# Performance work log

Measured on AMD Instinct MI355X. Metric: run time of the kernel, lower is better.

## Reference

```python
import jax, jax.numpy as jnp
import numpy as np

N_NODES = 50000
N_REL = 4
N_EDGES = 800000
IN_DIM = 128
HID = 128
N_CLASSES = 16


def setup_inputs() -> dict:
    key = jax.random.key(0)
    ks = jax.random.split(key, 12)
    feat = jax.random.normal(ks[0], (N_NODES, IN_DIM), dtype=jnp.float32)
    src = jax.random.randint(ks[1], (N_REL, N_EDGES), 0, N_NODES, dtype=jnp.int32)
    dst = jax.random.randint(ks[2], (N_REL, N_EDGES), 0, N_NODES, dtype=jnp.int32)
    s = 0.05
    W1 = jax.random.normal(ks[3], (N_REL, IN_DIM, HID), dtype=jnp.float32) * s
    b1 = jax.random.normal(ks[4], (N_REL, HID), dtype=jnp.float32) * s
    W2 = jax.random.normal(ks[5], (N_REL, HID, HID), dtype=jnp.float32) * s
    b2 = jax.random.normal(ks[6], (N_REL, HID), dtype=jnp.float32) * s
    W3 = jax.random.normal(ks[7], (N_REL, HID, HID), dtype=jnp.float32) * s
    b3 = jax.random.normal(ks[8], (N_REL, HID), dtype=jnp.float32) * s
    Wlin = jax.random.normal(ks[9], (HID, N_CLASSES), dtype=jnp.float32) * s
    blin = jax.random.normal(ks[10], (N_CLASSES,), dtype=jnp.float32) * s
    return {"feat": feat, "src": src, "dst": dst, "W1": W1, "b1": b1,
            "W2": W2, "b2": b2, "W3": W3, "b3": b3, "Wlin": Wlin, "blin": blin}


def _graph_conv(x, s, d, W, b, n_nodes):
    """DGL GraphConv with norm='both': D_dst^-1/2 * A * D_src^-1/2 * x, then @W + b."""
    ones = jnp.ones(s.shape[0], dtype=x.dtype)
    deg_out = jnp.maximum(jax.ops.segment_sum(ones, s, num_segments=n_nodes), 1.0)
    deg_in = jnp.maximum(jax.ops.segment_sum(ones, d, num_segments=n_nodes), 1.0)
    xs = x * (deg_out ** -0.5)[:, None]          # [N, F]
    agg = jax.ops.segment_sum(xs[s], d, num_segments=n_nodes)  # gather+scatter [N, F]
    agg = agg * (deg_in ** -0.5)[:, None]
    return agg @ W + b


def _hetero_layer(x, src, dst, W, b, n_nodes):
    # HeteroGraphConv aggregate='sum' over relations (loop over small fixed R)
    out = _graph_conv(x, src[0], dst[0], W[0], b[0], n_nodes)
    for r in range(1, src.shape[0]):
        out = out + _graph_conv(x, src[r], dst[r], W[r], b[r], n_nodes)
    return out


def _l2_normalize(x, eps=1e-12):
    # torch F.normalize: x / max(||x||_2, eps), per row
    nrm = jnp.sqrt(jnp.sum(x * x, axis=1, keepdims=True))
    return x / jnp.maximum(nrm, eps)


def reference(feat, src, dst, W1, b1, W2, b2, W3, b3, Wlin, blin):
    n = feat.shape[0]
    h = _hetero_layer(feat, src, dst, W1, b1, n)
    h = jax.nn.leaky_relu(_l2_normalize(h), negative_slope=0.01)
    h = _hetero_layer(h, src, dst, W2, b2, n)
    h = jax.nn.leaky_relu(_l2_normalize(h), negative_slope=0.01)
    h = _hetero_layer(h, src, dst, W3, b3, n)
    # update_all(copy_u, sum) across all relations (unnormalized scatter-sum)
    pooled = jax.ops.segment_sum(h[src[0]], dst[0], num_segments=n)
    for r in range(1, src.shape[0]):
        pooled = pooled + jax.ops.segment_sum(h[src[r]], dst[r], num_segments=n)
    hg = jnp.mean(pooled, axis=0, keepdims=True)  # dgl.mean_nodes -> [1, HID]
    return jax.nn.sigmoid(hg @ Wlin + blin)       # [1, n_classes]
```

## Files before the change

### kernel.cpp

```cpp
#include <hip/hip_runtime.h>
#include <hip/hip_bf16.h>

constexpr int N_NODES = 50000;
constexpr int N_REL   = 4;
constexpr int N_EDGES = 800000;
constexpr int DIM     = 128;
constexpr int N_CLS   = 16;

constexpr int CHUNK  = 256;
constexpr int NCHUNK = (N_NODES + CHUNK - 1) / CHUNK;
constexpr int NPART  = N_REL * NCHUNK;

constexpr int NCBR  = (N_NODES + 255) / 256;
constexpr int NCB   = N_REL * NCBR;
constexpr int TILE  = 8000;
constexpr int TPR   = N_EDGES / TILE;
constexpr int MAXB  = 6144;

constexpr int RNG    = 12544;
constexpr int NRANGE = 4;
constexpr int DTILE  = 80000;
constexpr int DNT    = N_EDGES / DTILE;

constexpr int NPB = 8;

constexpr float YSCALE = 32.0f;

typedef __attribute__((ext_vector_type(8))) short short8;
typedef __attribute__((ext_vector_type(4))) float float4v;
typedef __attribute__((ext_vector_type(2))) float floatx2;

__device__ __forceinline__ unsigned int f2bf_bits(float f) {
  unsigned int u = __float_as_uint(f);
  return (u + 0x7fffu + ((u >> 16) & 1u)) >> 16;
}
__device__ __forceinline__ unsigned int pack2bf(float a, float b) {
  return f2bf_bits(a) | (f2bf_bits(b) << 16);
}

__device__ __forceinline__ int LCOL(int p) { return (p & 7) * 16 + (p >> 3); }

__global__ __launch_bounds__(256) void degree_hist(
    const int* __restrict__ src, const int* __restrict__ dst,
    int* __restrict__ cnt_out, int* __restrict__ cnt_in) {
  int b = blockIdx.x;
  int t     = b % DNT;    b /= DNT;
  int range = b % NRANGE; b /= NRANGE;
  int r     = b % N_REL;  b /= N_REL;
  int which = b;
  const int* arr = (which ? dst : src) + (size_t)r * N_EDGES + (size_t)t * DTILE;
  int* cnt = (which ? cnt_in : cnt_out) + r * N_NODES;
  int tid = threadIdx.x;
  __shared__ int h[RNG];
  for (int i = tid; i < RNG; i += 256) h[i] = 0;
  __syncthreads();
  int lo = range * RNG;
  int hi = lo + RNG;
  const int4* a4 = (const int4*)arr;
  for (int i = tid; i < DTILE / 4; i += 256) {
    int4 v = a4[i];
    if (v.x >= lo && v.x < hi) atomicAdd(&h[v.x - lo], 1);
    if (v.y >= lo && v.y < hi) atomicAdd(&h[v.y - lo], 1);
    if (v.z >= lo && v.z < hi) atomicAdd(&h[v.z - lo], 1);
    if (v.w >= lo && v.w < hi) atomicAdd(&h[v.w - lo], 1);
  }
  __syncthreads();
  for (int i = tid; i < RNG; i += 256) {
    int n = lo + i;
    int c = h[i];
    if (n < N_NODES && c) atomicAdd(&cnt[n], c);
  }
}

__global__ __launch_bounds__(256) void scan_partial(
    const int* __restrict__ cnt_in, int* __restrict__ partial) {
  int b = blockIdx.x;
  int r = b / NCHUNK, c = b % NCHUNK;
  int i = c * CHUNK + threadIdx.x;
  int v = (i < N_NODES) ? cnt_in[r * N_NODES + i] : 0;
#pragma unroll
  for (int off = 1; off < 64; off <<= 1) v += __shfl_xor(v, off, 64);
  __shared__ int ws[4];
  if ((threadIdx.x & 63) == 0) ws[threadIdx.x >> 6] = v;
  __syncthreads();
  if (threadIdx.x == 0) partial[b] = ws[0] + ws[1] + ws[2] + ws[3];
}

__global__ __launch_bounds__(1024) void scan_offsets(
    const int* __restrict__ partial, int* __restrict__ chunk_off,
    int* __restrict__ row_ptr) {
  __shared__ int lds[1024];
  __shared__ int sexcl[1024];
  __shared__ int stotal;
  int tid = threadIdx.x;
  int v = (tid < NPART) ? partial[tid] : 0;
  lds[tid] = v;
  __syncthreads();
  for (int off = 1; off < 1024; off <<= 1) {
    int t = (tid >= off) ? lds[tid - off] : 0;
    __syncthreads();
    lds[tid] += t;
    __syncthreads();
  }
  int excl = lds[tid] - v;
  sexcl[tid] = excl;
  if (tid == NPART - 1) stotal = excl + v;
  if (tid < NPART) chunk_off[tid] = excl;
  __syncthreads();
  if (tid < N_REL) {
    int base = sexcl[tid * NCHUNK];
    int next = (tid < N_REL - 1) ? sexcl[(tid + 1) * NCHUNK] : stotal;
    row_ptr[tid * (N_NODES + 1) + N_NODES] = next - base;
  }
}

__global__ __launch_bounds__(256) void scan_expand(
    const int* __restrict__ cnt_in, const int* __restrict__ chunk_off,
    int* __restrict__ row_ptr, int* __restrict__ cbcur) {
  int b = blockIdx.x;
  int r = b / NCHUNK, c = b % NCHUNK;
  int tid = threadIdx.x;
  int i = c * CHUNK + tid;
  int v = (i < N_NODES) ? cnt_in[r * N_NODES + i] : 0;
  __shared__ int lds[CHUNK];
  lds[tid] = v;
  __syncthreads();
  for (int off = 1; off < CHUNK; off <<= 1) {
    int t = (tid >= off) ? lds[tid - off] : 0;
    __syncthreads();
    lds[tid] += t;
    __syncthreads();
  }
  int excl = lds[tid] - v;
  int base = chunk_off[b] - chunk_off[r * NCHUNK];
  if (i < N_NODES) row_ptr[r * (N_NODES + 1) + i] = base + excl;
  if (tid == 0) cbcur[r * NCBR + c] = base;
}

__global__ __launch_bounds__(256) void pass1_bin(
    const int* __restrict__ src, const int* __restrict__ dst,
    int* __restrict__ cbcur, unsigned int* __restrict__ binned) {
  int b = blockIdx.x;
  int r = b / TPR, t = b % TPR;
  const int* sp = src + (size_t)r * N_EDGES + t * TILE;
  const int* dp = dst + (size_t)r * N_EDGES + t * TILE;
  unsigned int* outp = binned + (size_t)r * N_EDGES;
  int tid = threadIdx.x;
  __shared__ int hist[NCBR];
  __shared__ int scanb[256];
  __shared__ int gbase[NCBR];
  __shared__ int lcur[NCBR];
  for (int i = tid; i < NCBR; i += 256) hist[i] = 0;
  __syncthreads();
  for (int i = tid; i < TILE; i += 256) atomicAdd(&hist[dp[i] >> 8], 1);
  __syncthreads();
  int v = (tid < NCBR) ? hist[tid] : 0;
  scanb[tid] = v;
  __syncthreads();
  for (int off = 1; off < 256; off <<= 1) {
    int tv = (tid >= off) ? scanb[tid - off] : 0;
    __syncthreads();
    scanb[tid] += tv;
    __syncthreads();
  }
  if (tid < NCBR) {
    int excl = scanb[tid] - v;
    gbase[tid] = atomicAdd(&cbcur[r * NCBR + tid], v) - excl;
    lcur[tid] = excl;
  }
  __syncthreads();
  for (int i = tid; i < TILE; i += 256) {
    int d = dp[i];
    int s = sp[i];
    int cb = d >> 8;
    int lp = atomicAdd(&lcur[cb], 1);
    outp[gbase[cb] + lp] = ((unsigned)s << 8) | (unsigned)(d & 255);
  }
}

__global__ __launch_bounds__(256) void pass2_sort(
    const unsigned int* __restrict__ binned, const int* __restrict__ row_ptr,
    unsigned short* __restrict__ csr) {
  int b = blockIdx.x;
  int r = b / NCBR, c = b % NCBR;
  int node0 = c * 256;
  int node1 = min(node0 + 256, N_NODES);
  int start = row_ptr[r * (N_NODES + 1) + node0];
  int endv  = row_ptr[r * (N_NODES + 1) + node1];
  int count = endv - start;
  const unsigned int* bp = binned + (size_t)r * N_EDGES + start;
  unsigned short* outg = csr + (size_t)r * N_EDGES + start;
  int tid = threadIdx.x;
  __shared__ int hist[4096];
  __shared__ int scanb[256];
  __shared__ unsigned short outb[MAXB];
  for (int i = tid; i < 4096; i += 256) hist[i] = 0;
  __syncthreads();
  for (int i = tid; i < count; i += 256) {
    unsigned int p = bp[i];
    unsigned int key = ((p & 255u) << 4) | ((p >> 8) >> 12);
    atomicAdd(&hist[key], 1);
  }
  __syncthreads();
  int t16 = tid * 16;
  int a[16];
  int tsum = 0;
#pragma unroll
  for (int j = 0; j < 16; ++j) { a[j] = hist[t16 + j]; tsum += a[j]; }
  scanb[tid] = tsum;
  __syncthreads();
  for (int off = 1; off < 256; off <<= 1) {
    int tv = (tid >= off) ? scanb[tid - off] : 0;
    __syncthreads();
    scanb[tid] += tv;
    __syncthreads();
  }
  int run = scanb[tid] - tsum;
#pragma unroll
  for (int j = 0; j < 16; ++j) { hist[t16 + j] = run; run += a[j]; }
  __syncthreads();
  if (count <= MAXB) {
    for (int i = tid; i < count; i += 256) {
      unsigned int p = bp[i];
      unsigned int s = p >> 8;
      unsigned int key = ((p & 255u) << 4) | (s >> 12);
      int pos = atomicAdd(&hist[key], 1);
      outb[pos] = (unsigned short)s;
    }
    __syncthreads();
    for (int i = tid; i < count; i += 256) outg[i] = outb[i];
  } else {
    for (int i = tid; i < count; i += 256) {
      unsigned int p = bp[i];
      unsigned int s = p >> 8;
      unsigned int key = ((p & 255u) << 4) | (s >> 12);
      int pos = atomicAdd(&hist[key], 1);
      outg[pos] = (unsigned short)s;
    }
  }
}

__global__ __launch_bounds__(256) void scales_kernel(
    const int* __restrict__ cnt_out, const int* __restrict__ cnt_in,
    float* __restrict__ soutF, float* __restrict__ sinF,
    float* __restrict__ wout) {
  int total = N_REL * N_NODES;
  for (int idx = blockIdx.x * blockDim.x + threadIdx.x; idx < total;
       idx += gridDim.x * blockDim.x) {
    soutF[idx] = YSCALE / sqrtf((float)max(cnt_out[idx], 1));
    sinF [idx] = (1.0f / YSCALE) / sqrtf((float)max(cnt_in[idx], 1));
  }
  for (int v = blockIdx.x * blockDim.x + threadIdx.x; v < N_NODES;
       v += gridDim.x * blockDim.x) {
    wout[v] = (float)(cnt_out[v] + cnt_out[N_NODES + v] +
                      cnt_out[2 * N_NODES + v] + cnt_out[3 * N_NODES + v]);
  }
}

__global__ __launch_bounds__(256) void cvt_feat_bf16(
    const float* __restrict__ in, unsigned short* __restrict__ outw, int n4) {
  int i = blockIdx.x * blockDim.x + threadIdx.x;
  if (i < n4) {
    float4 v = ((const float4*)in)[i];
    uint2 o;
    o.x = pack2bf(v.x, v.y);
    o.y = pack2bf(v.z, v.w);
    *(uint2*)(outw + (size_t)i * 4) = o;
  }
}

template <int PERMK>
__global__ __launch_bounds__(256) void prep_w(
    const float* __restrict__ W, const float* __restrict__ b,
    unsigned short* __restrict__ Wt, float* __restrict__ bsum) {
  int i = blockIdx.x * blockDim.x + threadIdx.x;
  if (i < N_REL * DIM * DIM) {
    int col = i >> 7, p = i & 127;
    int k = PERMK ? LCOL(p) : p;
    int rrel = col >> 7, n = col & 127;
    Wt[i] = (unsigned short)f2bf_bits(W[rrel * DIM * DIM + k * DIM + n]);
  }
  if (i < DIM) {
    int Lp = LCOL(i);
    bsum[i] = b[Lp] + b[DIM + Lp] + b[2 * DIM + Lp] + b[3 * DIM + Lp];
  }
}

__global__ __launch_bounds__(256) void gemm_y(
    const unsigned short* __restrict__ X, const unsigned short* __restrict__ Wt,
    const float* __restrict__ soutF, unsigned char* __restrict__ Yb) {
  int tid = threadIdx.x;
  int w   = tid >> 6;
  int l   = tid & 63;
  int l15 = l & 15, lq = l >> 4;
  int rowbase = blockIdx.x * 64;

  float4v acc[4][8] = {};
  const unsigned short* Wq = Wt + (size_t)(w * DIM) * DIM;

#pragma unroll
  for (int ks = 0; ks < 4; ++ks) {
    int k0 = ks * 32 + lq * 8;
    short8 bfr[8];
#pragma unroll
    for (int c = 0; c < 8; ++c)
      bfr[c] = *(const short8*)(Wq + (size_t)(c * 16 + l15) * DIM + k0);
#pragma unroll
    for (int i = 0; i < 4; ++i) {
      int rr = rowbase + i * 16 + l15;
      short8 afr = (rr < N_NODES)
          ? *(const short8*)(X + (size_t)rr * DIM + k0)
          : (short8)(short)0;
#pragma unroll
      for (int c = 0; c < 8; ++c)
        acc[i][c] = __builtin_amdgcn_mfma_f32_16x16x32_bf16(afr, bfr[c],
                                                            acc[i][c], 0, 0, 0);
    }
  }

  const float* so = soutF + (size_t)w * N_NODES;
  unsigned char* Yq = Yb + (size_t)w * N_NODES * DIM;
#pragma unroll
  for (int i = 0; i < 4; ++i) {
#pragma unroll
    for (int rr = 0; rr < 4; ++rr) {
      int grow = rowbase + i * 16 + lq * 4 + rr;
      if (grow < N_NODES) {
        float sc = so[grow];
        float v0 = acc[i][0][rr] * sc, v1 = acc[i][1][rr] * sc;
        float v2 = acc[i][2][rr] * sc, v3 = acc[i][3][rr] * sc;
        float v4 = acc[i][4][rr] * sc, v5 = acc[i][5][rr] * sc;
        float v6 = acc[i][6][rr] * sc, v7 = acc[i][7][rr] * sc;
        int t0 = __builtin_amdgcn_cvt_pk_fp8_f32(v0, v1, 0, false);
        t0 = __builtin_amdgcn_cvt_pk_fp8_f32(v2, v3, t0, true);
        int t1 = __builtin_amdgcn_cvt_pk_fp8_f32(v4, v5, 0, false);
        t1 = __builtin_amdgcn_cvt_pk_fp8_f32(v6, v7, t1, true);
        uint2 o;
        o.x = (unsigned)t0;
        o.y = (unsigned)t1;
        *(uint2*)(Yq + (size_t)grow * DIM + l15 * 8) = o;
      }
    }
  }
}

template <int MODE>
__global__ __launch_bounds__(256) void gather_y(
    const unsigned char* __restrict__ Yb, const unsigned short* __restrict__ csr,
    const int* __restrict__ row_ptr, const float* __restrict__ sinF,
    const float* __restrict__ bsum, void* __restrict__ out) {
  int d0   = blockIdx.x * NPB;
  int r    = threadIdx.x >> 6;
  int lane = threadIdx.x & 63;
  int g    = lane >> 4;
  int l16  = lane & 15;
  const unsigned short* cs = csr + (size_t)r * N_EDGES;
  const unsigned char*  Yq = Yb + (size_t)r * N_NODES * DIM;

  int rp = row_ptr[r * (N_NODES + 1) + d0 + min(lane, NPB)];

  __shared__ __align__(16) float lds[N_REL][NPB][132];

#pragma unroll 1
  for (int n = 0; n < NPB; ++n) {
    int beg = __shfl(rp, n, 64);
    int end = __shfl(rp, n + 1, 64);
    floatx2 acc[4];
#pragma unroll
    for (int j = 0; j < 4; ++j) acc[j] = (floatx2){0.f, 0.f};
    for (int e0 = beg; e0 < end; e0 += 16) {
      uint2 xr[4];
#pragma unroll
      for (int u = 0; u < 4; ++u) {
        int e = e0 + u * 4 + g;
        bool vv = e < end;
        int se = vv ? (int)cs[e] : 0;
        uint2 t = *(const uint2*)(Yq + (size_t)se * DIM + l16 * 8);
        xr[u].x = vv ? t.x : 0u;
        xr[u].y = vv ? t.y : 0u;
      }
#pragma unroll
      for (int u = 0; u < 4; ++u) {
        acc[0] += __builtin_amdgcn_cvt_pk_f32_fp8((int)xr[u].x, false);
        acc[1] += __builtin_amdgcn_cvt_pk_f32_fp8((int)xr[u].x, true);
        acc[2] += __builtin_amdgcn_cvt_pk_f32_fp8((int)xr[u].y, false);
        acc[3] += __builtin_amdgcn_cvt_pk_f32_fp8((int)xr[u].y, true);
      }
    }
#pragma unroll
    for (int j = 0; j < 4; ++j) {
      acc[j].x += __shfl_xor(acc[j].x, 16, 64);
      acc[j].y += __shfl_xor(acc[j].y, 16, 64);
      acc[j].x += __shfl_xor(acc[j].x, 32, 64);
      acc[j].y += __shfl_xor(acc[j].y, 32, 64);
    }
    if (g < 2) {
      float4 w;
      if (g == 0) w = make_float4(acc[0].x, acc[0].y, acc[1].x, acc[1].y);
      else        w = make_float4(acc[2].x, acc[2].y, acc[3].x, acc[3].y);
      *(float4*)&lds[r][n][l16 * 8 + g * 4] = w;
    }
  }
  __syncthreads();

  int nn = threadIdx.x >> 5;
  int ln = threadIdx.x & 31;
  int d  = d0 + nn;
  float s0 = sinF[d];
  float s1 = sinF[N_NODES + d];
  float s2 = sinF[2 * N_NODES + d];
  float s3 = sinF[3 * N_NODES + d];
  float4 a0 = *(const float4*)&lds[0][nn][ln * 4];
  float4 a1 = *(const float4*)&lds[1][nn][ln * 4];
  float4 a2 = *(const float4*)&lds[2][nn][ln * 4];
  float4 a3 = *(const float4*)&lds[3][nn][ln * 4];
  float4 bs = *(const float4*)&bsum[ln * 4];
  float v0 = s0 * a0.x + s1 * a1.x + s2 * a2.x + s3 * a3.x + bs.x;
  float v1 = s0 * a0.y + s1 * a1.y + s2 * a2.y + s3 * a3.y + bs.y;
  float v2 = s0 * a0.z + s1 * a1.z + s2 * a2.z + s3 * a3.z + bs.z;
  float v3 = s0 * a0.w + s1 * a1.w + s2 * a2.w + s3 * a3.w + bs.w;
  if (MODE == 1) {
    float ss = v0 * v0 + v1 * v1 + v2 * v2 + v3 * v3;
    ss += __shfl_xor(ss, 1, 32);
    ss += __shfl_xor(ss, 2, 32);
    ss += __shfl_xor(ss, 4, 32);
    ss += __shfl_xor(ss, 8, 32);
    ss += __shfl_xor(ss, 16, 32);
    float sc = 1.0f / fmaxf(sqrtf(ss), 1e-12f);
    v0 *= sc; v1 *= sc; v2 *= sc; v3 *= sc;
    v0 = v0 > 0.f ? v0 : 0.01f * v0;
    v1 = v1 > 0.f ? v1 : 0.01f * v1;
    v2 = v2 > 0.f ? v2 : 0.01f * v2;
    v3 = v3 > 0.f ? v3 : 0.01f * v3;
    uint2 o;
    o.x = pack2bf(v0, v1);
    o.y = pack2bf(v2, v3);
    *(uint2*)((unsigned short*)out + (size_t)d * DIM + ln * 4) = o;
  } else {
    float4 o = make_float4(v0, v1, v2, v3);
    *(float4*)((float*)out + (size_t)d * DIM + ln * 4) = o;
  }
}

__global__ __launch_bounds__(256) void pool_kernel(
    const float* __restrict__ h, const float* __restrict__ wout,
    float* __restrict__ hg) {
  int gw   = blockIdx.x * 4 + (threadIdx.x >> 6);
  int lane = threadIdx.x & 63;
  int nw   = gridDim.x * 4;
  float ax = 0.0f, ay = 0.0f;
  for (int v = gw; v < N_NODES; v += nw) {
    float w = wout[v];
    float2 hv = *(const float2*)(h + (size_t)v * DIM + lane * 2);
    ax = fmaf(w, hv.x, ax);
    ay = fmaf(w, hv.y, ay);
  }
  atomicAdd(&hg[lane * 2],     ax);
  atomicAdd(&hg[lane * 2 + 1], ay);
}

__global__ void head_kernel(const float* __restrict__ hg,
                            const float* __restrict__ Wlin,
                            const float* __restrict__ blin,
                            float* __restrict__ out) {
  int j = threadIdx.x;
  if (j < N_CLS) {
    float s = blin[j];
    const float invN = 1.0f / (float)N_NODES;
#pragma unroll 16
    for (int k = 0; k < DIM; ++k) {
      int Lk = (k & 7) * 16 + (k >> 3);
      s = fmaf(hg[k] * invN, Wlin[Lk * N_CLS + j], s);
    }
    out[j] = 1.0f / (1.0f + expf(-s));
  }
}

__global__ void fail_kernel(float* out) {
  int i = threadIdx.x;
  if (i < N_CLS) out[i] = 1e30f;
}

extern "C" void kernel_launch(void* const* d_in, const int* in_sizes, int n_in,
                              void* d_out, int out_size, void* d_ws, size_t ws_size,
                              hipStream_t stream) {
  const float* feat = (const float*)d_in[0];
  const int*   src  = (const int*)  d_in[1];
  const int*   dst  = (const int*)  d_in[2];
  const float* W1   = (const float*)d_in[3];
  const float* b1   = (const float*)d_in[4];
  const float* W2   = (const float*)d_in[5];
  const float* b2   = (const float*)d_in[6];
  const float* W3   = (const float*)d_in[7];
  const float* b3   = (const float*)d_in[8];
  const float* Wlin = (const float*)d_in[9];
  const float* blin = (const float*)d_in[10];
  float* out = (float*)d_out;

  char* base = (char*)d_ws;
  size_t off = 0;
  auto alloc = [&](size_t bytes) -> void* {
    void* q = base + off;
    off = (off + bytes + 255) & ~(size_t)255;
    return q;
  };
  int*   cnt_out  = (int*)  alloc((size_t)N_REL * N_NODES * 4);
  int*   cnt_in   = (int*)  alloc((size_t)N_REL * N_NODES * 4);
  int*   row_ptr  = (int*)  alloc((size_t)N_REL * (N_NODES + 1) * 4);
  float* soutF    = (float*)alloc((size_t)N_REL * N_NODES * 4);
  float* sinF     = (float*)alloc((size_t)N_REL * N_NODES * 4);
  float* wout     = (float*)alloc((size_t)N_NODES * 4);
  float* hg       = (float*)alloc((size_t)DIM * 4);
  int*   partial  = (int*)  alloc((size_t)NPART * 4);
  int*   chunkoff = (int*)  alloc((size_t)NPART * 4);
  int*   cbcur    = (int*)  alloc((size_t)NCB * 4);
  unsigned int*   binned = (unsigned int*)  alloc((size_t)N_REL * N_EDGES * 4);
  unsigned short* csr    = (unsigned short*)alloc((size_t)N_REL * N_EDGES * 2);
  unsigned char*  Yb     = (unsigned char*) alloc((size_t)N_REL * N_NODES * DIM);
  unsigned short* X0     = (unsigned short*)alloc((size_t)N_NODES * DIM * 2);
  unsigned short* X1     = (unsigned short*)alloc((size_t)N_NODES * DIM * 2);
  unsigned short* X2     = (unsigned short*)alloc((size_t)N_NODES * DIM * 2);
  float* H3       = (float*)alloc((size_t)N_NODES * DIM * 4);
  unsigned short* Wt1 = (unsigned short*)alloc((size_t)N_REL * DIM * DIM * 2);
  unsigned short* Wt2 = (unsigned short*)alloc((size_t)N_REL * DIM * DIM * 2);
  unsigned short* Wt3 = (unsigned short*)alloc((size_t)N_REL * DIM * DIM * 2);
  float* bs1 = (float*)alloc(DIM * 4);
  float* bs2 = (float*)alloc(DIM * 4);
  float* bs3 = (float*)alloc(DIM * 4);

  if (off > ws_size) {
    fail_kernel<<<1, 64, 0, stream>>>(out);
    return;
  }

  hipMemsetAsync(cnt_out, 0, (size_t)2 * N_REL * N_NODES * 4, stream);
  hipMemsetAsync(hg, 0, DIM * 4, stream);

  degree_hist  <<<2 * N_REL * NRANGE * DNT, 256, 0, stream>>>(src, dst, cnt_out, cnt_in);
  scan_partial <<<NPART, 256, 0, stream>>>(cnt_in, partial);
  scan_offsets <<<1, 1024, 0, stream>>>(partial, chunkoff, row_ptr);
  scan_expand  <<<NPART, 256, 0, stream>>>(cnt_in, chunkoff, row_ptr, cbcur);
  pass1_bin    <<<N_REL * TPR, 256, 0, stream>>>(src, dst, cbcur, binned);
  pass2_sort   <<<NCB, 256, 0, stream>>>(binned, row_ptr, csr);
  scales_kernel<<<512, 256, 0, stream>>>(cnt_out, cnt_in, soutF, sinF, wout);

  cvt_feat_bf16<<<(N_NODES * DIM / 4 + 255) / 256, 256, 0, stream>>>(
      feat, X0, N_NODES * DIM / 4);
  prep_w<0><<<(N_REL * DIM * DIM + 255) / 256, 256, 0, stream>>>(W1, b1, Wt1, bs1);
  prep_w<1><<<(N_REL * DIM * DIM + 255) / 256, 256, 0, stream>>>(W2, b2, Wt2, bs2);
  prep_w<1><<<(N_REL * DIM * DIM + 255) / 256, 256, 0, stream>>>(W3, b3, Wt3, bs3);

  int gemm_blocks = (N_NODES + 63) / 64;
  int gath_blocks = (N_NODES + NPB - 1) / NPB;

  gemm_y     <<<gemm_blocks, 256, 0, stream>>>(X0, Wt1, soutF, Yb);
  gather_y<1><<<gath_blocks, 256, 0, stream>>>(Yb, csr, row_ptr, sinF, bs1, X1);
  gemm_y     <<<gemm_blocks, 256, 0, stream>>>(X1, Wt2, soutF, Yb);
  gather_y<1><<<gath_blocks, 256, 0, stream>>>(Yb, csr, row_ptr, sinF, bs2, X2);
  gemm_y     <<<gemm_blocks, 256, 0, stream>>>(X2, Wt3, soutF, Yb);
  gather_y<0><<<gath_blocks, 256, 0, stream>>>(Yb, csr, row_ptr, sinF, bs3, H3);

  pool_kernel<<<256, 256, 0, stream>>>(H3, wout, hg);
  head_kernel<<<1, 64, 0, stream>>>(hg, Wlin, blin, out);
}
```

Baseline: 563.0 us.

## Pack degree histogram into 16-bit LDS counters and interleave gather across four nodes

The degree histogram now packs two 16-bit counts per 32-bit LDS word so all 50000 nodes fit in one block's shared memory. This drops the four-way range split that forced every block to re-read its edge tile four times, and halves the tile size. The gather kernel stages each block's CSR source indices in LDS when they fit (up to 512), then processes four destination nodes at once with interleaved loads to raise memory-level parallelism. Costs are more registers and LDS per block, a risk of 16-bit count overflow for very high-degree tiles, and divergence when the four nodes have unequal degrees.

```diff
diff --git a/kernel.cpp b/kernel.cpp
--- a/kernel.cpp
+++ b/kernel.cpp
@@ -17,12 +17,12 @@
 constexpr int TPR   = N_EDGES / TILE;
 constexpr int MAXB  = 6144;
 
-constexpr int RNG    = 12544;
-constexpr int NRANGE = 4;
-constexpr int DTILE  = 80000;
+constexpr int RNGW   = 25088;
+constexpr int DTILE  = 40000;
 constexpr int DNT    = N_EDGES / DTILE;
 
 constexpr int NPB = 8;
+constexpr int CAP = 512;
 
 constexpr float YSCALE = 32.0f;
 
@@ -45,30 +45,29 @@
     int* __restrict__ cnt_out, int* __restrict__ cnt_in) {
   int b = blockIdx.x;
   int t     = b % DNT;    b /= DNT;
-  int range = b % NRANGE; b /= NRANGE;
   int r     = b % N_REL;  b /= N_REL;
   int which = b;
   const int* arr = (which ? dst : src) + (size_t)r * N_EDGES + (size_t)t * DTILE;
   int* cnt = (which ? cnt_in : cnt_out) + r * N_NODES;
   int tid = threadIdx.x;
-  __shared__ int h[RNG];
-  for (int i = tid; i < RNG; i += 256) h[i] = 0;
-  __syncthreads();
-  int lo = range * RNG;
-  int hi = lo + RNG;
+  __shared__ unsigned int h[RNGW];
+  for (int i = tid; i < RNGW; i += 256) h[i] = 0;
+  __syncthreads();
   const int4* a4 = (const int4*)arr;
   for (int i = tid; i < DTILE / 4; i += 256) {
     int4 v = a4[i];
-    if (v.x >= lo && v.x < hi) atomicAdd(&h[v.x - lo], 1);
-    if (v.y >= lo && v.y < hi) atomicAdd(&h[v.y - lo], 1);
-    if (v.z >= lo && v.z < hi) atomicAdd(&h[v.z - lo], 1);
-    if (v.w >= lo && v.w < hi) atomicAdd(&h[v.w - lo], 1);
-  }
-  __syncthreads();
-  for (int i = tid; i < RNG; i += 256) {
-    int n = lo + i;
-    int c = h[i];
-    if (n < N_NODES && c) atomicAdd(&cnt[n], c);
+    atomicAdd(&h[v.x >> 1], 1u << ((v.x & 1) * 16));
+    atomicAdd(&h[v.y >> 1], 1u << ((v.y & 1) * 16));
+    atomicAdd(&h[v.z >> 1], 1u << ((v.z & 1) * 16));
+    atomicAdd(&h[v.w >> 1], 1u << ((v.w & 1) * 16));
+  }
+  __syncthreads();
+  for (int i = tid; i < N_NODES / 2; i += 256) {
+    unsigned int w = h[i];
+    if (!w) continue;
+    unsigned int c0 = w & 0xffffu, c1 = w >> 16;
+    if (c0) atomicAdd(&cnt[2 * i], (int)c0);
+    if (c1) atomicAdd(&cnt[2 * i + 1], (int)c1);
   }
 }
 
@@ -358,49 +357,86 @@
   const unsigned char*  Yq = Yb + (size_t)r * N_NODES * DIM;
 
   int rp = row_ptr[r * (N_NODES + 1) + d0 + min(lane, NPB)];
-
+  int beg0 = __shfl(rp, 0, 64);
+  int cnt  = __shfl(rp, NPB, 64) - beg0;
+
+  __shared__ unsigned short scsr[N_REL][CAP];
   __shared__ __align__(16) float lds[N_REL][NPB][132];
 
+  int ccap = min(cnt, CAP);
+  for (int i = lane; i < ccap; i += 64) scsr[r][i] = cs[beg0 + i];
+
+  auto body = [&](auto CS) {
 #pragma unroll 1
-  for (int n = 0; n < NPB; ++n) {
-    int beg = __shfl(rp, n, 64);
-    int end = __shfl(rp, n + 1, 64);
-    floatx2 acc[4];
-#pragma unroll
-    for (int j = 0; j < 4; ++j) acc[j] = (floatx2){0.f, 0.f};
-    for (int e0 = beg; e0 < end; e0 += 16) {
-      uint2 xr[4];
-#pragma unroll
-      for (int u = 0; u < 4; ++u) {
-        int e = e0 + u * 4 + g;
-        bool vv = e < end;
-        int se = vv ? (int)cs[e] : 0;
-        uint2 t = *(const uint2*)(Yq + (size_t)se * DIM + l16 * 8);
-        xr[u].x = vv ? t.x : 0u;
-        xr[u].y = vv ? t.y : 0u;
+    for (int n = 0; n < NPB; n += 4) {
+      int bq[4], eq[4];
+#pragma unroll
+      for (int q = 0; q < 4; ++q) {
+        bq[q] = __shfl(rp, n + q, 64);
+        eq[q] = __shfl(rp, n + q + 1, 64);
       }
-#pragma unroll
-      for (int u = 0; u < 4; ++u) {
-        acc[0] += __builtin_amdgcn_cvt_pk_f32_fp8((int)xr[u].x, false);
-        acc[1] += __builtin_amdgcn_cvt_pk_f32_fp8((int)xr[u].x, true);
-        acc[2] += __builtin_amdgcn_cvt_pk_f32_fp8((int)xr[u].y, false);
-        acc[3] += __builtin_amdgcn_cvt_pk_f32_fp8((int)xr[u].y, true);
+      floatx2 ac[4][4];
+#pragma unroll
+      for (int q = 0; q < 4; ++q)
+#pragma unroll
+        for (int j = 0; j < 4; ++j) ac[q][j] = (floatx2){0.f, 0.f};
+      int pq[4] = {bq[0], bq[1], bq[2], bq[3]};
+      while (pq[0] < eq[0] || pq[1] < eq[1] || pq[2] < eq[2] || pq[3] < eq[3]) {
+        bool dq[4];
+        uint2 x[4][4];
+#pragma unroll
+        for (int q = 0; q < 4; ++q) {
+          dq[q] = pq[q] < eq[q];
+          if (dq[q]) {
+#pragma unroll
+            for (int u = 0; u < 4; ++u) {
+              int e = pq[q] + u * 4 + g;
+              bool vv = e < eq[q];
+              int se = (int)CS(min(e, eq[q] - 1));
+              uint2 t = *(const uint2*)(Yq + (size_t)se * DIM + l16 * 8);
+              x[q][u].x = vv ? t.x : 0u;
+              x[q][u].y = vv ? t.y : 0u;
+            }
+          }
+        }
+#pragma unroll
+        for (int q = 0; q < 4; ++q) {
+          if (dq[q]) {
+#pragma unroll
+            for (int u = 0; u < 4; ++u) {
+              ac[q][0] += __builtin_amdgcn_cvt_pk_f32_fp8((int)x[q][u].x, false);
+              ac[q][1] += __builtin_amdgcn_cvt_pk_f32_fp8((int)x[q][u].x, true);
+              ac[q][2] += __builtin_amdgcn_cvt_pk_f32_fp8((int)x[q][u].y, false);
+              ac[q][3] += __builtin_amdgcn_cvt_pk_f32_fp8((int)x[q][u].y, true);
+            }
+            pq[q] += 16;
+          }
+        }
+      }
+#pragma unroll
+      for (int q = 0; q < 4; ++q)
+#pragma unroll
+        for (int j = 0; j < 4; ++j) {
+          ac[q][j].x += __shfl_xor(ac[q][j].x, 16, 64);
+          ac[q][j].y += __shfl_xor(ac[q][j].y, 16, 64);
+          ac[q][j].x += __shfl_xor(ac[q][j].x, 32, 64);
+          ac[q][j].y += __shfl_xor(ac[q][j].y, 32, 64);
+        }
+      if (g < 2) {
+#pragma unroll
+        for (int q = 0; q < 4; ++q) {
+          float4 wv = (g == 0)
+              ? make_float4(ac[q][0].x, ac[q][0].y, ac[q][1].x, ac[q][1].y)
+              : make_float4(ac[q][2].x, ac[q][2].y, ac[q][3].x, ac[q][3].y);
+          *(float4*)&lds[r][n + q][l16 * 8 + g * 4] = wv;
+        }
       }
     }
-#pragma unroll
-    for (int j = 0; j < 4; ++j) {
-      acc[j].x += __shfl_xor(acc[j].x, 16, 64);
-      acc[j].y += __shfl_xor(acc[j].y, 16, 64);
-      acc[j].x += __shfl_xor(acc[j].x, 32, 64);
-      acc[j].y += __shfl_xor(acc[j].y, 32, 64);
-    }
-    if (g < 2) {
-      float4 w;
-      if (g == 0) w = make_float4(acc[0].x, acc[0].y, acc[1].x, acc[1].y);
-      else        w = make_float4(acc[2].x, acc[2].y, acc[3].x, acc[3].y);
-      *(float4*)&lds[r][n][l16 * 8 + g * 4] = w;
-    }
-  }
+  };
+  if (cnt <= CAP)
+    body([&](int e) { return scsr[r][e - beg0]; });
+  else
+    body([&](int e) { return cs[e]; });
   __syncthreads();
 
   int nn = threadIdx.x >> 5;
@@ -536,7 +572,7 @@
   hipMemsetAsync(cnt_out, 0, (size_t)2 * N_REL * N_NODES * 4, stream);
   hipMemsetAsync(hg, 0, DIM * 4, stream);
 
-  degree_hist  <<<2 * N_REL * NRANGE * DNT, 256, 0, stream>>>(src, dst, cnt_out, cnt_in);
+  degree_hist  <<<2 * N_REL * DNT, 256, 0, stream>>>(src, dst, cnt_out, cnt_in);
   scan_partial <<<NPART, 256, 0, stream>>>(cnt_in, partial);
   scan_offsets <<<1, 1024, 0, stream>>>(partial, chunkoff, row_ptr);
   scan_expand  <<<NPART, 256, 0, stream>>>(cnt_in, chunkoff, row_ptr, cbcur);
```

Measured after the change: 571.2 us. Within noise of the previous version (+1.5%).
